# Optimization experiments

Hardware: AMD Instinct MI355X
Metric: run time of the kernel (lower is better)

Reference implementation:

```python
import jax, jax.numpy as jnp
import numpy as np

B, H, W, C = 8, 56, 56, 384
HEADS, K, PAD = 12, 3, 1


def setup_inputs() -> dict:
    key = jax.random.key(0)
    k1, k2, k3, k4 = jax.random.split(key, 4)
    s = 1.0 / np.sqrt(C).astype(np.float32)
    return {
        "x": jax.random.normal(k1, (B, H, W, C), jnp.float32),
        "Wv": jax.random.normal(k2, (C, C), jnp.float32) * s,
        "Wa": jax.random.normal(k3, (K ** 4 * HEADS, C), jnp.float32) * s,
        "Wo": jax.random.normal(k4, (C, C), jnp.float32) * s,
    }


def reference(x, Wv, Wa, Wo):
    b, h, w, c = x.shape
    heads, k, pad = HEADS, K, PAD
    d = c // heads
    k2 = k * k
    n = h * w  # stride=1 -> pooled grid == input grid, AvgPool2d(1,1) is identity

    # value projection then unfold into k x k local windows (overlap via padding)
    v = jnp.einsum('bhwc,oc->bhwo', x, Wv)
    vp = jnp.pad(v, ((0, 0), (pad, pad), (pad, pad), (0, 0)))
    # (b, h, w, k2, c): window position p = i*k + j
    patches = jnp.stack([vp[:, i:i + h, j:j + w] for i in range(k) for j in range(k)], axis=3)
    v_unf = patches.reshape(b, n, k2, heads, d)

    a = jnp.einsum('bhwc,oc->bhwo', x, Wa).reshape(b, n, heads, k2, k2)
    attn = jax.nn.softmax(a * (d ** -0.5), axis=-1)  # (b, n, heads, k2, k2)

    # weighted combination of window values
    out = jnp.einsum('bnhpq,bnqhd->bnphd', attn, v_unf).reshape(b, h, w, k2, c)

    # fold: overlap-add each window position back onto the padded canvas
    canvas = jnp.zeros((b, h + 2 * pad, w + 2 * pad, c), x.dtype)
    p = 0
    for i in range(k):
        for j in range(k):
            canvas = canvas.at[:, i:i + h, j:j + w].add(out[:, :, :, p])
            p += 1
    y = canvas[:, pad:pad + h, pad:pad + w]

    return jnp.einsum('bhwc,oc->bhwo', y, Wo)
```

## Files before the change

kernel.cpp:

```cpp
#include <hip/hip_runtime.h>
#include <hip/hip_bf16.h>

#define B_ 8
#define H_ 56
#define W_ 56
#define C_ 384
#define HEADS_ 12
#define NPIX (B_*H_*W_)
#define NPAD 1408
#define KDIM 384

typedef unsigned short u16;
typedef __attribute__((ext_vector_type(4))) float f32x4;
typedef __attribute__((ext_vector_type(8))) short bf16x8;
typedef __attribute__((ext_vector_type(8))) unsigned short u16x8;

#define GLDS16(g, l)                                                            \
    __builtin_amdgcn_global_load_lds(                                           \
        (const __attribute__((address_space(1))) void*)(g),                     \
        (__attribute__((address_space(3))) void*)(l), 16, 0, 0)

__device__ __forceinline__ float bf2f(u16 u) {
    union { unsigned int uu; float f; } cv; cv.uu = ((unsigned)u) << 16; return cv.f;
}
__device__ __forceinline__ u16 f2bf(float f) {
    __hip_bfloat16 hb = __float2bfloat16(f);
    return *reinterpret_cast<u16*>(&hb);
}

__global__ void pack_kernel(const float* __restrict__ x, const float* __restrict__ Wv,
                            const float* __restrict__ Wa, const float* __restrict__ Wo,
                            u16* __restrict__ xb, __hip_bfloat16* __restrict__ wcat,
                            __hip_bfloat16* __restrict__ wob) {
    const int NX8 = NPIX * C_ / 8;
    const int NW = NPAD * KDIM;
    const int NO = C_ * C_;
    const int total = NX8 + NW + NO;
    for (int idx = blockIdx.x * blockDim.x + threadIdx.x; idx < total;
         idx += gridDim.x * blockDim.x) {
        if (idx < NX8) {
            float4 a = ((const float4*)x)[idx * 2];
            float4 b = ((const float4*)x)[idx * 2 + 1];
            u16x8 o;
            o[0] = f2bf(a.x); o[1] = f2bf(a.y); o[2] = f2bf(a.z); o[3] = f2bf(a.w);
            o[4] = f2bf(b.x); o[5] = f2bf(b.y); o[6] = f2bf(b.z); o[7] = f2bf(b.w);
            ((u16x8*)xb)[idx] = o;
        } else if (idx < NX8 + NW) {
            int t = idx - NX8;
            int o = t / KDIM;
            float v = 0.f;
            if (o < 384) v = Wv[t];
            else if (o < 1356) v = Wa[t - 147456];
            wcat[t] = __float2bfloat16(v);
        } else {
            int t = idx - NX8 - NW;
            wob[t] = __float2bfloat16(Wo[t]);
        }
    }
}


#define STAGE(buf_, kt_) do {                                                        \
    _Pragma("unroll") for (int c = 0; c < 4; ++c) {                                  \
        int rowA = (wid * 4 + c) * 8 + srow;                                         \
        int scol = (sslot ^ (rowA & 7)) * 8;                                         \
        GLDS16(&A[(size_t)(bm * 128 + rowA) * K + (kt_) + scol],                     \
               &As[buf_][(wid * 4 + c) * 512]);                                      \
        GLDS16(&Bw[(size_t)(bn * 128 + rowA) * K + (kt_) + scol],                    \
               &Bs[buf_][(wid * 4 + c) * 512]);                                      \
    } } while (0)

template<int OUT_BF16>
__global__ __launch_bounds__(256) void gemm_bt(const u16* __restrict__ A, const u16* __restrict__ Bw,
                                               void* __restrict__ Cout, int N, int K,
                                               int gridN, int q, int r) {
    __shared__ u16 As[2][128 * 64];
    __shared__ u16 Bs[2][128 * 64];
    const int bid = blockIdx.x;
    const int xcd = bid & 7, ii = bid >> 3;
    const int logical = (xcd < r) ? xcd * (q + 1) + ii : r * (q + 1) + (xcd - r) * q + ii;
    const int bm = logical / gridN, bn = logical - bm * gridN;
    const int tid = threadIdx.x;
    const int lane = tid & 63, wid = tid >> 6;
    const int wm = wid >> 1, wn = wid & 1;
    const int fr = lane & 15;
    const int kg = lane >> 4;
    const int srow = lane >> 3;
    const int sslot = lane & 7;
    const int NT = K >> 6;
    f32x4 acc[4][4] = {};

    STAGE(0, 0);
    __syncthreads();
    for (int t = 0; t < NT; ++t) {
        const int cur = t & 1;
        if (t + 1 < NT) STAGE((t + 1) & 1, (t + 1) * 64);
#pragma unroll
        for (int ks = 0; ks < 2; ++ks) {
            bf16x8 af[4], bfr[4];
#pragma unroll
            for (int m = 0; m < 4; ++m) {
                int row = wm * 64 + m * 16 + fr;
                int slot = (ks * 4 + kg) ^ (row & 7);
                af[m] = *(const bf16x8*)(&As[cur][row * 64 + slot * 8]);
            }
#pragma unroll
            for (int n = 0; n < 4; ++n) {
                int row = wn * 64 + n * 16 + fr;
                int slot = (ks * 4 + kg) ^ (row & 7);
                bfr[n] = *(const bf16x8*)(&Bs[cur][row * 64 + slot * 8]);
            }
#pragma unroll
            for (int m = 0; m < 4; ++m)
#pragma unroll
                for (int n = 0; n < 4; ++n)
                    acc[m][n] = __builtin_amdgcn_mfma_f32_16x16x32_bf16(af[m], bfr[n], acc[m][n], 0, 0, 0);
        }
        __syncthreads();
    }
    const int r0 = bm * 128 + wm * 64 + kg * 4;
    const int c0 = bn * 128 + wn * 64 + fr;
#pragma unroll
    for (int m = 0; m < 4; ++m)
#pragma unroll
        for (int n = 0; n < 4; ++n)
#pragma unroll
            for (int j = 0; j < 4; ++j) {
                size_t off = (size_t)(r0 + m * 16 + j) * N + (c0 + n * 16);
                if (OUT_BF16) ((__hip_bfloat16*)Cout)[off] = __float2bfloat16(acc[m][n][j]);
                else          ((float*)Cout)[off] = acc[m][n][j];
            }
}

__global__ __launch_bounds__(384) void attn_fold(const __hip_bfloat16* __restrict__ va,
                                                 __hip_bfloat16* __restrict__ yb) {
    __shared__ float wls[8][300];
    const int tid = threadIdx.x;
    const int bid = blockIdx.x;
    const int b = bid & 7;
    const int bi = bid >> 3;
    const int rs0 = bi * 8;
    const u16* vap = (const u16*)va;

    if (tid < 96) {
        const int pixL = tid / 12, h = tid - pixL * 12;
        const int rs = rs0 + pixL;
        const int r = rs / 56, s = rs - r * 56;
        float w[25];
#pragma unroll
        for (int t = 0; t < 25; ++t) w[t] = 0.f;
        const float SC = 0.17677669529663687f;
#pragma unroll
        for (int i = 0; i < 3; ++i) {
            int cy = r + 1 - i;
            if ((unsigned)cy >= (unsigned)H_) continue;
#pragma unroll
            for (int j = 0; j < 3; ++j) {
                int cx = s + 1 - j;
                if ((unsigned)cx >= (unsigned)W_) continue;
                const u16* ap = vap + (size_t)(b * 3136 + cy * 56 + cx) * NPAD + C_ + h * 81 + (i * 3 + j) * 9;
                float aq[9];
                float mx = -1e30f;
#pragma unroll
                for (int qq = 0; qq < 9; ++qq) { aq[qq] = bf2f(ap[qq]); mx = fmaxf(mx, aq[qq]); }
                float ssum = 0.f;
#pragma unroll
                for (int qq = 0; qq < 9; ++qq) { aq[qq] = __expf((aq[qq] - mx) * SC); ssum += aq[qq]; }
                float inv = 1.f / ssum;
#pragma unroll
                for (int qi = 0; qi < 3; ++qi)
#pragma unroll
                    for (int qj = 0; qj < 3; ++qj)
                        w[(qi - i + 2) * 5 + (qj - j + 2)] += aq[qi * 3 + qj] * inv;
            }
        }
#pragma unroll
        for (int t = 0; t < 25; ++t) wls[pixL][t * 12 + h] = w[t];
    }
    __syncthreads();

    {
        const int g = tid / 48, t = tid - g * 48;
        const int c0 = t * 8, hh = t >> 2;
        const int rs = rs0 + g;
        const int r = rs / 56, s = rs - r * 56;
        float acc[8];
#pragma unroll
        for (int e = 0; e < 8; ++e) acc[e] = 0.f;
        const float* wp = &wls[g][hh];
#pragma unroll
        for (int dy = -2; dy <= 2; ++dy) {
            int py = r + dy;
            if ((unsigned)py >= (unsigned)H_) continue;
#pragma unroll
            for (int dx = -2; dx <= 2; ++dx) {
                int px = s + dx;
                if ((unsigned)px >= (unsigned)W_) continue;
                float w = wp[((dy + 2) * 5 + (dx + 2)) * 12];
                u16x8 v = *(const u16x8*)(vap + (size_t)(b * 3136 + py * 56 + px) * NPAD + c0);
#pragma unroll
                for (int e = 0; e < 8; ++e) acc[e] += w * bf2f(v[e]);
            }
        }
        u16x8 o;
#pragma unroll
        for (int e = 0; e < 8; ++e) o[e] = f2bf(acc[e]);
        *(u16x8*)((u16*)yb + (size_t)(b * 3136 + rs) * C_ + c0) = o;
    }
}

extern "C" void kernel_launch(void* const* d_in, const int* in_sizes, int n_in,
                              void* d_out, int out_size, void* d_ws, size_t ws_size,
                              hipStream_t stream) {
    const float* x  = (const float*)d_in[0];
    const float* Wv = (const float*)d_in[1];
    const float* Wa = (const float*)d_in[2];
    const float* Wo = (const float*)d_in[3];
    char* ws = (char*)d_ws;
    u16*            xb   = (u16*)(ws);
    __hip_bfloat16* wcat = (__hip_bfloat16*)(ws + 19267584);
    __hip_bfloat16* wob  = (__hip_bfloat16*)(ws + 20348928);
    __hip_bfloat16* va   = (__hip_bfloat16*)(ws + 20643840);
    __hip_bfloat16* yb   = (__hip_bfloat16*)(ws + 91291648);

    hipLaunchKernelGGL(pack_kernel, dim3(2048), dim3(256), 0, stream,
                       x, Wv, Wa, Wo, xb, wcat, wob);

    {
        int gridN = NPAD / 128, nwg = (NPIX / 128) * gridN;
        int q = nwg / 8, r = nwg % 8;
        hipLaunchKernelGGL(HIP_KERNEL_NAME(gemm_bt<1>), dim3(nwg), dim3(256), 0, stream,
                           (const u16*)xb, (const u16*)wcat, (void*)va, NPAD, KDIM, gridN, q, r);
    }
    hipLaunchKernelGGL(attn_fold, dim3(NPIX / 8), dim3(384), 0, stream, va, yb);
    {
        int gridN = C_ / 128, nwg = (NPIX / 128) * gridN;
        int q = nwg / 8, r = nwg % 8;
        hipLaunchKernelGGL(HIP_KERNEL_NAME(gemm_bt<0>), dim3(nwg), dim3(256), 0, stream,
                           (const u16*)yb, (const u16*)wob, d_out, C_, KDIM, gridN, q, r);
    }
}
```

Measured before the change: 121.4 us.

## Single-buffer GEMM LDS tiles and spread attention softmax over all threads

The GEMM drops its double-buffered LDS staging in favour of one buffer loaded and synchronised at each k-step. This halves shared memory per block, which may allow more resident blocks, but it gives up the overlap of global loads with MFMA work. In attn_fold, the per-window softmax now runs as 864 independent tasks spread over all 384 threads instead of 96 threads each doing nine windows. The results are accumulated into zero-initialised LDS through atomicAdd, which adds an extra barrier and atomic contention.

```diff
diff --git a/kernel.cpp b/kernel.cpp
--- a/kernel.cpp
+++ b/kernel.cpp
@@ -59,23 +59,12 @@
     }
 }
 
-
-#define STAGE(buf_, kt_) do {                                                        \
-    _Pragma("unroll") for (int c = 0; c < 4; ++c) {                                  \
-        int rowA = (wid * 4 + c) * 8 + srow;                                         \
-        int scol = (sslot ^ (rowA & 7)) * 8;                                         \
-        GLDS16(&A[(size_t)(bm * 128 + rowA) * K + (kt_) + scol],                     \
-               &As[buf_][(wid * 4 + c) * 512]);                                      \
-        GLDS16(&Bw[(size_t)(bn * 128 + rowA) * K + (kt_) + scol],                    \
-               &Bs[buf_][(wid * 4 + c) * 512]);                                      \
-    } } while (0)
-
 template<int OUT_BF16>
 __global__ __launch_bounds__(256) void gemm_bt(const u16* __restrict__ A, const u16* __restrict__ Bw,
                                                void* __restrict__ Cout, int N, int K,
                                                int gridN, int q, int r) {
-    __shared__ u16 As[2][128 * 64];
-    __shared__ u16 Bs[2][128 * 64];
+    __shared__ u16 As[128 * 64];
+    __shared__ u16 Bs[128 * 64];
     const int bid = blockIdx.x;
     const int xcd = bid & 7, ii = bid >> 3;
     const int logical = (xcd < r) ? xcd * (q + 1) + ii : r * (q + 1) + (xcd - r) * q + ii;
@@ -87,14 +76,16 @@
     const int kg = lane >> 4;
     const int srow = lane >> 3;
     const int sslot = lane & 7;
-    const int NT = K >> 6;
     f32x4 acc[4][4] = {};
-
-    STAGE(0, 0);
-    __syncthreads();
-    for (int t = 0; t < NT; ++t) {
-        const int cur = t & 1;
-        if (t + 1 < NT) STAGE((t + 1) & 1, (t + 1) * 64);
+    for (int kt = 0; kt < K; kt += 64) {
+#pragma unroll
+        for (int c = 0; c < 4; ++c) {
+            int rowA = (wid * 4 + c) * 8 + srow;
+            int scol = (sslot ^ srow) * 8;
+            GLDS16(&A[(size_t)(bm * 128 + rowA) * K + kt + scol], &As[(wid * 4 + c) * 512]);
+            GLDS16(&Bw[(size_t)(bn * 128 + rowA) * K + kt + scol], &Bs[(wid * 4 + c) * 512]);
+        }
+        __syncthreads();
 #pragma unroll
         for (int ks = 0; ks < 2; ++ks) {
             bf16x8 af[4], bfr[4];
@@ -102,13 +93,13 @@
             for (int m = 0; m < 4; ++m) {
                 int row = wm * 64 + m * 16 + fr;
                 int slot = (ks * 4 + kg) ^ (row & 7);
-                af[m] = *(const bf16x8*)(&As[cur][row * 64 + slot * 8]);
+                af[m] = *(const bf16x8*)(&As[row * 64 + slot * 8]);
             }
 #pragma unroll
             for (int n = 0; n < 4; ++n) {
                 int row = wn * 64 + n * 16 + fr;
                 int slot = (ks * 4 + kg) ^ (row & 7);
-                bfr[n] = *(const bf16x8*)(&Bs[cur][row * 64 + slot * 8]);
+                bfr[n] = *(const bf16x8*)(&Bs[row * 64 + slot * 8]);
             }
 #pragma unroll
             for (int m = 0; m < 4; ++m)
@@ -141,41 +132,34 @@
     const int bi = bid >> 3;
     const int rs0 = bi * 8;
     const u16* vap = (const u16*)va;
-
-    if (tid < 96) {
-        const int pixL = tid / 12, h = tid - pixL * 12;
-        const int rs = rs0 + pixL;
-        const int r = rs / 56, s = rs - r * 56;
-        float w[25];
-#pragma unroll
-        for (int t = 0; t < 25; ++t) w[t] = 0.f;
-        const float SC = 0.17677669529663687f;
-#pragma unroll
-        for (int i = 0; i < 3; ++i) {
-            int cy = r + 1 - i;
-            if ((unsigned)cy >= (unsigned)H_) continue;
-#pragma unroll
-            for (int j = 0; j < 3; ++j) {
-                int cx = s + 1 - j;
-                if ((unsigned)cx >= (unsigned)W_) continue;
-                const u16* ap = vap + (size_t)(b * 3136 + cy * 56 + cx) * NPAD + C_ + h * 81 + (i * 3 + j) * 9;
-                float aq[9];
-                float mx = -1e30f;
-#pragma unroll
-                for (int qq = 0; qq < 9; ++qq) { aq[qq] = bf2f(ap[qq]); mx = fmaxf(mx, aq[qq]); }
-                float ssum = 0.f;
-#pragma unroll
-                for (int qq = 0; qq < 9; ++qq) { aq[qq] = __expf((aq[qq] - mx) * SC); ssum += aq[qq]; }
-                float inv = 1.f / ssum;
-#pragma unroll
-                for (int qi = 0; qi < 3; ++qi)
-#pragma unroll
-                    for (int qj = 0; qj < 3; ++qj)
-                        w[(qi - i + 2) * 5 + (qj - j + 2)] += aq[qi * 3 + qj] * inv;
-            }
-        }
-#pragma unroll
-        for (int t = 0; t < 25; ++t) wls[pixL][t * 12 + h] = w[t];
+    const float SC = 0.17677669529663687f;
+
+    for (int i = tid; i < 2400; i += 384) ((float*)wls)[i] = 0.f;
+    __syncthreads();
+
+    for (int task = tid; task < 864; task += 384) {
+        int pixL = task / 108, rem = task - pixL * 108;
+        int h = rem / 9, ij = rem - h * 9;
+        int i = ij / 3, j = ij - i * 3;
+        int rs = rs0 + pixL;
+        int r = rs / 56, s = rs - r * 56;
+        int cy = r + 1 - i, cx = s + 1 - j;
+        if ((unsigned)cy >= (unsigned)H_ || (unsigned)cx >= (unsigned)W_) continue;
+        const u16* ap = vap + (size_t)(b * 3136 + cy * 56 + cx) * NPAD + C_ + h * 81 + ij * 9;
+        float aq[9];
+        float mx = -1e30f;
+#pragma unroll
+        for (int qq = 0; qq < 9; ++qq) { aq[qq] = bf2f(ap[qq]); mx = fmaxf(mx, aq[qq]); }
+        float ssum = 0.f;
+#pragma unroll
+        for (int qq = 0; qq < 9; ++qq) { aq[qq] = __expf((aq[qq] - mx) * SC); ssum += aq[qq]; }
+        float inv = 1.f / ssum;
+#pragma unroll
+        for (int qi = 0; qi < 3; ++qi)
+#pragma unroll
+            for (int qj = 0; qj < 3; ++qj)
+                atomicAdd(&wls[pixL][((qi - i + 2) * 5 + (qj - j + 2)) * 12 + h],
+                          aq[qi * 3 + qj] * inv);
     }
     __syncthreads();
 
```

After: 216.0 us. 1.78x slower.
